# Kernel optimization log

Hardware: AMD Instinct MI355X
Metric: run time of the kernel (lower is better)

Reference implementation:

```python
import jax, jax.numpy as jnp
import numpy as np

N = 2048
VOTE_THRESH = 0.65
SOFT_TH = 0.05      # INFERENCE_TH in the original
MAX_DET = 100       # cfg.TEST.DETECTIONS_PER_IMAGE
NUM_CLASSES = 80


def setup_inputs() -> dict:
    key = jax.random.key(0)
    k1, k2, k3, k4 = jax.random.split(key, 4)
    xy = jax.random.uniform(k1, (N, 2), dtype=jnp.float32) * 800.0
    wh = jax.random.uniform(k2, (N, 2), dtype=jnp.float32) * 196.0 + 4.0
    boxes = jnp.concatenate([xy, xy + wh], axis=1)          # valid x1y1x2y2 boxes
    scores = jax.random.uniform(k3, (N,), dtype=jnp.float32) * 0.95 + 0.05
    labels = jax.random.randint(k4, (N,), 0, NUM_CLASSES, dtype=jnp.int32)
    return {"boxes": boxes, "scores": scores, "labels": labels}


def _bbox_vote_soft(det):
    """Faithful fixed-shape version of bbox_vote(..., vote_type='soft_vote').
    det: (n, 6) = [x1, y1, x2, y2, score, label]. Returns (MAX_DET, 6) rows + valid mask."""
    n = det.shape[0]
    BUF = 2 * n + 1                      # each det yields <=1 soft row + <=1 merged row; last slot = trash
    order = jnp.argsort(-det[:, 4])
    det = det[order]
    area = (det[:, 2] - det[:, 0]) * (det[:, 3] - det[:, 1])

    def step(state, _):
        alive, buf, cnt = state
        any_alive = jnp.any(alive)
        pos = jnp.argmax(alive)          # first alive in score-sorted order == current top det
        cur = det[pos]
        xx1 = jnp.maximum(cur[0], det[:, 0])
        yy1 = jnp.maximum(cur[1], det[:, 1])
        xx2 = jnp.minimum(cur[2], det[:, 2])
        yy2 = jnp.minimum(cur[3], det[:, 3])
        inter = jnp.clip(xx2 - xx1, 0.0) * jnp.clip(yy2 - yy1, 0.0)
        iou = inter / (area[pos] + area - inter)
        merge = alive & (iou >= VOTE_THRESH)
        n_merge = merge.sum()
        s = det[:, 4]
        ms = jnp.where(merge, s, 0.0)
        wsum = ms.sum()
        wsafe = jnp.where(wsum > 0, wsum, 1.0)          # guard masked no-op iterations
        wbox = (det[:, :4] * ms[:, None]).sum(0) / wsafe  # score-weighted box merge
        maxs = jnp.max(ms)                               # max score among merged (scores > 0)
        row0 = jnp.concatenate([wbox, maxs[None], cur[5][None]])  # == single det when n_merge==1
        soft_s = s * (1.0 - iou)                         # soft-NMS decayed scores
        soft_valid = merge & (soft_s >= SOFT_TH) & (n_merge > 1)
        soft_rows = jnp.concatenate([det[:, :4], soft_s[:, None], det[:, 5:6]], axis=1)
        valid = jnp.concatenate([any_alive[None], soft_valid])
        rows = jnp.concatenate([row0[None], soft_rows], axis=0)   # (n+1, 6)
        idxs = jnp.where(valid, cnt + jnp.cumsum(valid) - 1, BUF - 1)
        buf = buf.at[idxs].set(rows)
        cnt = cnt + valid.sum()
        alive = alive & (iou < VOTE_THRESH)              # drop all merged dets
        return (alive, buf, cnt), None

    init = (jnp.ones((n,), bool), jnp.zeros((BUF, 6), det.dtype), jnp.int32(0))
    (alive, buf, cnt), _ = jax.lax.scan(step, init, None, length=n)
    res = buf[: BUF - 1]
    valid = jnp.arange(BUF - 1) < cnt
    sc = jnp.where(valid, res[:, 4], -jnp.inf)
    keep = jnp.argsort(-sc)[:MAX_DET]                    # final sort by score desc + truncate
    return res[keep], valid[keep]


def reference(boxes, scores, labels):
    labf = labels.astype(boxes.dtype)
    maxc = boxes.max() + 1.0                             # batched-NMS class-offset trick
    det = jnp.concatenate([boxes + labf[:, None] * maxc, scores[:, None], labf[:, None]], axis=1)
    out, valid = _bbox_vote_soft(det)
    ob = jnp.where(valid[:, None], out[:, :4] - out[:, 5:6] * maxc, 0.0)
    os_ = jnp.where(valid, out[:, 4], 0.0)
    ol = jnp.where(valid, out[:, 5], 0.0)
    return ob, os_, ol
```

## Files before the change

kernel.cpp:

```cpp
#include <hip/hip_runtime.h>

#define NCLS 80
#define VOTE_TH 0.65f
#define SOFT_THR 0.05f
#define MAXDET 100
#define NB 1281
#define BINBASE 31232
#define CANDCAP 512
#define SEG 21
#define LAST_Z  19
#define LAST_P  ((int)0xAAAAAABDu)

#define ST(p, v) __hip_atomic_store((p), (v), __ATOMIC_RELAXED, __HIP_MEMORY_SCOPE_AGENT)
#define LD(p)    __hip_atomic_load((p), __ATOMIC_RELAXED, __HIP_MEMORY_SCOPE_AGENT)

__device__ __forceinline__ int bin_of(unsigned int b) {
    int bin = (int)(b >> 15) - BINBASE;
    return bin < 0 ? 0 : (bin > NB - 1 ? NB - 1 : bin);
}

__global__ __launch_bounds__(256, 1) void nms_fused(
    const float* __restrict__ boxes,
    const float* __restrict__ scores,
    const int* __restrict__ labels,
    int* __restrict__ kCnt,
    float* __restrict__ sArrG,
    float* __restrict__ rows,
    float* __restrict__ out,
    int n)
{
#pragma clang fp contract(off)
    const int tid = threadIdx.x;
    const int lane = tid & 63;
    const int wave = tid >> 6;
    const int cls = blockIdx.x * 4 + wave;
    const unsigned long long lmask = (1ull << lane) - 1ull;

    __shared__ int   labLds[2048];
    __shared__ int   uidx[4][64];
    __shared__ float redmax[4];
    __shared__ int   oldSh;
    __shared__ int   cnts[NCLS];
    __shared__ int   hist[NB];
    __shared__ unsigned long long cand[CANDCAP];
    __shared__ int   ncand_sh, T_sh, K_sh, tot_sh;

    const float4* b4 = (const float4*)boxes;
    float4 v[8];
#pragma unroll
    for (int i = 0; i < 8; ++i) {
        int idx = tid + i * 256;
        v[i] = (idx < n) ? b4[idx]
                         : make_float4(-3.0e38f, -3.0e38f, -3.0e38f, -3.0e38f);
    }
    int lab[8];
#pragma unroll
    for (int i = 0; i < 8; ++i) {
        int idx = tid + i * 256;
        lab[i] = (idx < n) ? labels[idx] : -1;
    }
    float m = -3.0e38f;
#pragma unroll
    for (int i = 0; i < 8; ++i)
        m = fmaxf(m, fmaxf(fmaxf(v[i].x, v[i].y), fmaxf(v[i].z, v[i].w)));
#pragma unroll
    for (int d = 32; d; d >>= 1) m = fmaxf(m, __shfl_xor(m, d));
    if (lane == 0) redmax[wave] = m;
#pragma unroll
    for (int i = 0; i < 8; ++i) labLds[tid + i * 256] = lab[i];
    __syncthreads();

    const float maxc = fmaxf(fmaxf(redmax[0], redmax[1]),
                             fmaxf(redmax[2], redmax[3])) + 1.0f;
    const float off = (float)cls * maxc;
    const float cls_f = (float)cls;

    int myLab[32];
#pragma unroll
    for (int c = 0; c < 32; ++c) myLab[c] = labLds[c * 64 + lane];
    int k = 0;
#pragma unroll 4
    for (int c = 0; c < 32; ++c) {
        bool p = (myLab[c] == cls);
        unsigned long long b = __ballot(p);
        if (p) {
            int w = k + __popcll(b & lmask);
            if (w < 64) uidx[wave][w] = c * 64 + lane;
        }
        k += __popcll(b);
    }
    if (k > 64) k = 64;
    __syncthreads();

    float s = 0.0f;
    float4 bb = make_float4(0.f, 0.f, 0.f, 0.f);
    if (lane < k) {
        int gi = uidx[wave][lane];
        s = scores[gi];
        bb = b4[gi];
    }

    int r = 0;
#pragma unroll
    for (int j = 0; j < 64; ++j) {
        float sj = __shfl(s, j);
        r += ((sj > s) || (sj == s && j < lane)) ? 1 : 0;
    }
    float x1 = 0.f, y1 = 0.f, x2 = 0.f, y2 = 0.f;
    if (lane < k) {
        x1 = bb.x + off; y1 = bb.y + off;
        x2 = bb.z + off; y2 = bb.w + off;
    }
    int addr = r * 4;
    x1 = __int_as_float(__builtin_amdgcn_ds_permute(addr, __float_as_int(x1)));
    y1 = __int_as_float(__builtin_amdgcn_ds_permute(addr, __float_as_int(y1)));
    x2 = __int_as_float(__builtin_amdgcn_ds_permute(addr, __float_as_int(x2)));
    y2 = __int_as_float(__builtin_amdgcn_ds_permute(addr, __float_as_int(y2)));
    s  = __int_as_float(__builtin_amdgcn_ds_permute(addr, __float_as_int(s)));

    float area = (x2 - x1) * (y2 - y1);
    bool alive = lane < k;

    float* rbase = rows + cls * 64 * 6;
    float* sbase = sArrG + cls * 64;
    int lcnt = 0;
    while (true) {
        unsigned long long avm = __ballot(alive);
        if (avm == 0ull) break;
        int pos = (int)__builtin_ctzll(avm);

        float cx1 = __shfl(x1, pos), cy1 = __shfl(y1, pos);
        float cx2 = __shfl(x2, pos), cy2 = __shfl(y2, pos);
        float carea = __shfl(area, pos), cs = __shfl(s, pos);

        float xx1 = fmaxf(cx1, x1), yy1 = fmaxf(cy1, y1);
        float xx2 = fminf(cx2, x2), yy2 = fminf(cy2, y2);
        float inter = fmaxf(xx2 - xx1, 0.0f) * fmaxf(yy2 - yy1, 0.0f);
        float iou = inter / ((carea + area) - inter);

        bool merge = alive && (iou >= VOTE_TH);
        unsigned long long mb = __ballot(merge);
        int nm = __popcll(mb);

        if (nm == 1) {
            if (lane == 0) {
                float* rp = rbase + lcnt * 6;
                ST(&rp[0], (cx1 * cs) / cs);
                ST(&rp[1], (cy1 * cs) / cs);
                ST(&rp[2], (cx2 * cs) / cs);
                ST(&rp[3], (cy2 * cs) / cs);
                ST(&rp[4], cs);
                ST(&rp[5], cls_f);
                ST(&sbase[lcnt], cs);
            }
            lcnt += 1;
        } else {
            float msv = merge ? s : 0.0f;
            float w0 = msv, w1 = x1 * msv, w2 = y1 * msv, w3 = x2 * msv, w4 = y2 * msv;
#pragma unroll
            for (int d = 32; d; d >>= 1) {
                w0 += __shfl_xor(w0, d);
                w1 += __shfl_xor(w1, d);
                w2 += __shfl_xor(w2, d);
                w3 += __shfl_xor(w3, d);
                w4 += __shfl_xor(w4, d);
            }
            float soft = s * (1.0f - iou);
            bool sv = merge && (soft >= SOFT_THR);
            unsigned long long sb = __ballot(sv);
            int nsoft = __popcll(sb);
            if (lane == 0) {
                float* rp = rbase + lcnt * 6;
                ST(&rp[0], w1 / w0);
                ST(&rp[1], w2 / w0);
                ST(&rp[2], w3 / w0);
                ST(&rp[3], w4 / w0);
                ST(&rp[4], cs);
                ST(&rp[5], cls_f);
                ST(&sbase[lcnt], cs);
            }
            if (sv) {
                int wp = lcnt + 1 + __popcll(sb & lmask);
                float* rp = rbase + wp * 6;
                ST(&rp[0], x1);
                ST(&rp[1], y1);
                ST(&rp[2], x2);
                ST(&rp[3], y2);
                ST(&rp[4], soft);
                ST(&rp[5], cls_f);
                ST(&sbase[wp], soft);
            }
            lcnt += 1 + nsoft;
        }
        alive = alive && (iou < VOTE_TH);
    }

    if (lane == 0) ST(&kCnt[cls], lcnt);

    __threadfence();
    __syncthreads();
    if (tid == 0)
        oldSh = __hip_atomic_fetch_add((int*)out, 1, __ATOMIC_ACQ_REL,
                                       __HIP_MEMORY_SCOPE_AGENT);
    __syncthreads();
    const int old = oldSh;
    if (old != LAST_Z && old != LAST_P) return;

    for (int i = tid; i < 6 * MAXDET; i += 256) out[i] = 0.0f;
    if (tid < NCLS) cnts[tid] = LD(&kCnt[tid]);
    for (int i = tid; i < NB; i += 256) hist[i] = 0;
    if (tid == 0) { ncand_sh = 0; tot_sh = 0; }
    __syncthreads();

    if (tid < NCLS) atomicAdd(&tot_sh, cnts[tid]);
    float svals[20];
    {
        int ci = 0;
        for (int c = wave; c < NCLS; c += 4, ++ci) {
            float sv = 0.0f;
            if (lane < cnts[c]) {
                sv = LD(&sArrG[c * 64 + lane]);
                atomicAdd(&hist[bin_of(__float_as_uint(sv))], 1);
            }
            svals[ci] = sv;
        }
    }
    __syncthreads();

    if (tid < 64) {
        int cnt_total = tot_sh;
        int K = (cnt_total < MAXDET) ? cnt_total : MAXDET;
        if (lane == 0) K_sh = K;
        int part = 0;
        if (lane < 61) {
            int b0 = lane * SEG;
            for (int b = b0; b < b0 + SEG; ++b) part += hist[b];
        }
        int suf = part;
#pragma unroll
        for (int d = 1; d < 64; d <<= 1) {
            int vsh = __shfl_down(suf, d);
            if (lane + d < 64) suf += vsh;
        }
        unsigned long long bm = __ballot(suf >= K);
        int L = (bm != 0ull) ? (63 - __builtin_clzll(bm)) : 0;
        if (lane == L) {
            int acc = suf - part;
            int T = 0;
            for (int b = L * SEG + SEG - 1; b >= L * SEG; --b) {
                acc += hist[b];
                if (acc >= K) { T = b; break; }
            }
            T_sh = T;
        }
    }
    __syncthreads();
    const int K = K_sh;
    if (K <= 0) return;
    const int T = T_sh;

    {
        int ci = 0;
        for (int c = wave; c < NCLS; c += 4, ++ci) {
            if (lane < cnts[c]) {
                unsigned int sb = __float_as_uint(svals[ci]);
                if (bin_of(sb) >= T) {
                    int idx = c * 64 + lane;
                    int p = atomicAdd(&ncand_sh, 1);
                    if (p < CANDCAP)
                        cand[p] = ((unsigned long long)sb << 32) |
                                  (unsigned long long)(0xFFFFFFFFu - (unsigned int)idx);
                }
            }
        }
    }
    __syncthreads();

    int nc = ncand_sh; if (nc > CANDCAP) nc = CANDCAP;
    for (int j = tid; j < nc; j += 256) {
        unsigned long long my = cand[j];
        int rank = 0;
        for (int l = 0; l < nc; ++l) rank += (cand[l] > my) ? 1 : 0;
        if (rank < K) {
            int idx = (int)(0xFFFFFFFFu - (unsigned int)(my & 0xFFFFFFFFull));
            float* rp = rows + idx * 6;
            float r0 = LD(&rp[0]);
            float r1 = LD(&rp[1]);
            float r2 = LD(&rp[2]);
            float r3 = LD(&rp[3]);
            float r4 = LD(&rp[4]);
            float lb = LD(&rp[5]);
            float o = lb * maxc;
            out[rank * 4 + 0] = r0 - o;
            out[rank * 4 + 1] = r1 - o;
            out[rank * 4 + 2] = r2 - o;
            out[rank * 4 + 3] = r3 - o;
            out[4 * MAXDET + rank] = r4;
            out[5 * MAXDET + rank] = lb;
        }
    }
}

extern "C" void kernel_launch(void* const* d_in, const int* in_sizes, int n_in,
                              void* d_out, int out_size, void* d_ws, size_t ws_size,
                              hipStream_t stream) {
    const float* boxes  = (const float*)d_in[0];
    const float* scores = (const float*)d_in[1];
    const int*   labels = (const int*)d_in[2];
    float* out = (float*)d_out;
    const int n = in_sizes[1];

    char* ws = (char*)d_ws;
    int*   kCnt  = (int*)(ws + 0);
    float* sArrG = (float*)(ws + 512);
    float* rows  = (float*)(ws + 512 + 20480);

    hipLaunchKernelGGL(nms_fused, dim3(NCLS / 4), dim3(256), 0, stream,
                       boxes, scores, labels, kCnt, sArrG, rows, out, n);
}
```

Measured before the change: 92.47 us.

## Stage per-class rows in LDS and pre-select per-block top-100 before global merge

Vote output rows and scores are now written to shared memory instead of global workspace with per-element atomic stores. Each block then ranks its own 256 candidates locally and publishes only its top 100 keys plus packed 64-bit row data to global memory. The last block reads these compact keys directly, avoiding per-class count loads and scattered row fetches. This adds a local 256-way rank pass per block and changes the workspace layout.

```diff
diff --git a/kernel.cpp b/kernel.cpp
--- a/kernel.cpp
+++ b/kernel.cpp
@@ -8,24 +8,30 @@
 #define BINBASE 31232
 #define CANDCAP 512
 #define SEG 21
+#define NBLK 20
 #define LAST_Z  19
 #define LAST_P  ((int)0xAAAAAABDu)
 
-#define ST(p, v) __hip_atomic_store((p), (v), __ATOMIC_RELAXED, __HIP_MEMORY_SCOPE_AGENT)
-#define LD(p)    __hip_atomic_load((p), __ATOMIC_RELAXED, __HIP_MEMORY_SCOPE_AGENT)
+#define STU(p, v) __hip_atomic_store((p), (v), __ATOMIC_RELAXED, __HIP_MEMORY_SCOPE_AGENT)
+#define LDU(p)    __hip_atomic_load((p), __ATOMIC_RELAXED, __HIP_MEMORY_SCOPE_AGENT)
+
+typedef unsigned long long u64;
 
 __device__ __forceinline__ int bin_of(unsigned int b) {
     int bin = (int)(b >> 15) - BINBASE;
     return bin < 0 ? 0 : (bin > NB - 1 ? NB - 1 : bin);
 }
+__device__ __forceinline__ u64 packf(float a, float b) {
+    return (u64)__float_as_uint(a) | ((u64)__float_as_uint(b) << 32);
+}
 
 __global__ __launch_bounds__(256, 1) void nms_fused(
     const float* __restrict__ boxes,
     const float* __restrict__ scores,
     const int* __restrict__ labels,
-    int* __restrict__ kCnt,
-    float* __restrict__ sArrG,
-    float* __restrict__ rows,
+    u64* __restrict__ keyG,
+    u64* __restrict__ candG,
+    int* __restrict__ rowTot,
     float* __restrict__ out,
     int n)
 {
@@ -39,10 +45,14 @@
     __shared__ int   labLds[2048];
     __shared__ int   uidx[4][64];
     __shared__ float redmax[4];
+    __shared__ float rowsL[4 * 64 * 6];
+    __shared__ float sL[4 * 64];
+    __shared__ int   lcntL[4];
+    __shared__ u64   keysL[256];
     __shared__ int   oldSh;
-    __shared__ int   cnts[NCLS];
     __shared__ int   hist[NB];
-    __shared__ unsigned long long cand[CANDCAP];
+    __shared__ u64   cand[CANDCAP];
+    __shared__ short candPos[CANDCAP];
     __shared__ int   ncand_sh, T_sh, K_sh, tot_sh;
 
     const float4* b4 = (const float4*)boxes;
@@ -121,8 +131,8 @@
     float area = (x2 - x1) * (y2 - y1);
     bool alive = lane < k;
 
-    float* rbase = rows + cls * 64 * 6;
-    float* sbase = sArrG + cls * 64;
+    float* rbase = rowsL + wave * 64 * 6;
+    float* sbase = sL + wave * 64;
     int lcnt = 0;
     while (true) {
         unsigned long long avm = __ballot(alive);
@@ -145,13 +155,10 @@
         if (nm == 1) {
             if (lane == 0) {
                 float* rp = rbase + lcnt * 6;
-                ST(&rp[0], (cx1 * cs) / cs);
-                ST(&rp[1], (cy1 * cs) / cs);
-                ST(&rp[2], (cx2 * cs) / cs);
-                ST(&rp[3], (cy2 * cs) / cs);
-                ST(&rp[4], cs);
-                ST(&rp[5], cls_f);
-                ST(&sbase[lcnt], cs);
+                rp[0] = (cx1 * cs) / cs; rp[1] = (cy1 * cs) / cs;
+                rp[2] = (cx2 * cs) / cs; rp[3] = (cy2 * cs) / cs;
+                rp[4] = cs; rp[5] = cls_f;
+                sbase[lcnt] = cs;
             }
             lcnt += 1;
         } else {
@@ -171,31 +178,49 @@
             int nsoft = __popcll(sb);
             if (lane == 0) {
                 float* rp = rbase + lcnt * 6;
-                ST(&rp[0], w1 / w0);
-                ST(&rp[1], w2 / w0);
-                ST(&rp[2], w3 / w0);
-                ST(&rp[3], w4 / w0);
-                ST(&rp[4], cs);
-                ST(&rp[5], cls_f);
-                ST(&sbase[lcnt], cs);
+                rp[0] = w1 / w0; rp[1] = w2 / w0;
+                rp[2] = w3 / w0; rp[3] = w4 / w0;
+                rp[4] = cs; rp[5] = cls_f;
+                sbase[lcnt] = cs;
             }
             if (sv) {
                 int wp = lcnt + 1 + __popcll(sb & lmask);
                 float* rp = rbase + wp * 6;
-                ST(&rp[0], x1);
-                ST(&rp[1], y1);
-                ST(&rp[2], x2);
-                ST(&rp[3], y2);
-                ST(&rp[4], soft);
-                ST(&rp[5], cls_f);
-                ST(&sbase[wp], soft);
+                rp[0] = x1; rp[1] = y1; rp[2] = x2; rp[3] = y2;
+                rp[4] = soft; rp[5] = cls_f;
+                sbase[wp] = soft;
             }
             lcnt += 1 + nsoft;
         }
         alive = alive && (iou < VOTE_TH);
     }
-
-    if (lane == 0) ST(&kCnt[cls], lcnt);
+    if (lane == 0) lcntL[wave] = lcnt;
+    __syncthreads();
+
+    const int nvalid = lcntL[0] + lcntL[1] + lcntL[2] + lcntL[3];
+    const bool valid = lane < lcntL[wave];
+    u64 mykey = 0ull;
+    if (valid) {
+        unsigned int sb = __float_as_uint(sL[wave * 64 + lane]);
+        int gidx = cls * 64 + lane;
+        mykey = ((u64)sb << 32) | (u64)(0xFFFFFFFFu - (unsigned int)gidx);
+    }
+    keysL[tid] = mykey;
+    __syncthreads();
+    int lrank = 0;
+    for (int j = 0; j < 256; ++j)
+        lrank += (keysL[j] > mykey) ? 1 : 0;
+    if (valid && lrank < 100) {
+        int base = blockIdx.x * 100 + lrank;
+        const float* rp = rowsL + (wave * 64 + lane) * 6;
+        STU(&keyG[base], mykey);
+        STU(&candG[base * 3 + 0], packf(rp[0], rp[1]));
+        STU(&candG[base * 3 + 1], packf(rp[2], rp[3]));
+        STU(&candG[base * 3 + 2], packf(rp[4], rp[5]));
+    }
+    if (tid >= nvalid && tid < 100)
+        STU(&keyG[blockIdx.x * 100 + tid], 0ull);
+    if (tid == 0) STU(&rowTot[blockIdx.x], nvalid);
 
     __threadfence();
     __syncthreads();
@@ -207,24 +232,21 @@
     if (old != LAST_Z && old != LAST_P) return;
 
     for (int i = tid; i < 6 * MAXDET; i += 256) out[i] = 0.0f;
-    if (tid < NCLS) cnts[tid] = LD(&kCnt[tid]);
     for (int i = tid; i < NB; i += 256) hist[i] = 0;
     if (tid == 0) { ncand_sh = 0; tot_sh = 0; }
-    __syncthreads();
-
-    if (tid < NCLS) atomicAdd(&tot_sh, cnts[tid]);
-    float svals[20];
-    {
-        int ci = 0;
-        for (int c = wave; c < NCLS; c += 4, ++ci) {
-            float sv = 0.0f;
-            if (lane < cnts[c]) {
-                sv = LD(&sArrG[c * 64 + lane]);
-                atomicAdd(&hist[bin_of(__float_as_uint(sv))], 1);
-            }
-            svals[ci] = sv;
-        }
-    }
+    u64 kv[8];
+#pragma unroll
+    for (int ii = 0; ii < 8; ++ii) {
+        int j = tid + ii * 256;
+        kv[ii] = (j < NBLK * 100) ? LDU(&keyG[j]) : 0ull;
+    }
+    int bt = (tid < NBLK) ? LDU(&rowTot[tid]) : 0;
+    __syncthreads();
+    if (tid < NBLK) atomicAdd(&tot_sh, bt);
+#pragma unroll
+    for (int ii = 0; ii < 8; ++ii)
+        if (kv[ii] != 0ull)
+            atomicAdd(&hist[bin_of((unsigned int)(kv[ii] >> 32))], 1);
     __syncthreads();
 
     if (tid < 64) {
@@ -259,18 +281,14 @@
     if (K <= 0) return;
     const int T = T_sh;
 
-    {
-        int ci = 0;
-        for (int c = wave; c < NCLS; c += 4, ++ci) {
-            if (lane < cnts[c]) {
-                unsigned int sb = __float_as_uint(svals[ci]);
-                if (bin_of(sb) >= T) {
-                    int idx = c * 64 + lane;
-                    int p = atomicAdd(&ncand_sh, 1);
-                    if (p < CANDCAP)
-                        cand[p] = ((unsigned long long)sb << 32) |
-                                  (unsigned long long)(0xFFFFFFFFu - (unsigned int)idx);
-                }
+#pragma unroll
+    for (int ii = 0; ii < 8; ++ii) {
+        if (kv[ii] != 0ull &&
+            bin_of((unsigned int)(kv[ii] >> 32)) >= T) {
+            int p = atomicAdd(&ncand_sh, 1);
+            if (p < CANDCAP) {
+                cand[p] = kv[ii];
+                candPos[p] = (short)(tid + ii * 256);
             }
         }
     }
@@ -278,18 +296,20 @@
 
     int nc = ncand_sh; if (nc > CANDCAP) nc = CANDCAP;
     for (int j = tid; j < nc; j += 256) {
-        unsigned long long my = cand[j];
+        u64 my = cand[j];
         int rank = 0;
         for (int l = 0; l < nc; ++l) rank += (cand[l] > my) ? 1 : 0;
         if (rank < K) {
-            int idx = (int)(0xFFFFFFFFu - (unsigned int)(my & 0xFFFFFFFFull));
-            float* rp = rows + idx * 6;
-            float r0 = LD(&rp[0]);
-            float r1 = LD(&rp[1]);
-            float r2 = LD(&rp[2]);
-            float r3 = LD(&rp[3]);
-            float r4 = LD(&rp[4]);
-            float lb = LD(&rp[5]);
+            int pos = (int)candPos[j];
+            u64 u0 = LDU(&candG[pos * 3 + 0]);
+            u64 u1 = LDU(&candG[pos * 3 + 1]);
+            u64 u2 = LDU(&candG[pos * 3 + 2]);
+            float r0 = __uint_as_float((unsigned int)(u0 & 0xFFFFFFFFull));
+            float r1 = __uint_as_float((unsigned int)(u0 >> 32));
+            float r2 = __uint_as_float((unsigned int)(u1 & 0xFFFFFFFFull));
+            float r3 = __uint_as_float((unsigned int)(u1 >> 32));
+            float r4 = __uint_as_float((unsigned int)(u2 & 0xFFFFFFFFull));
+            float lb = __uint_as_float((unsigned int)(u2 >> 32));
             float o = lb * maxc;
             out[rank * 4 + 0] = r0 - o;
             out[rank * 4 + 1] = r1 - o;
@@ -311,10 +331,10 @@
     const int n = in_sizes[1];
 
     char* ws = (char*)d_ws;
-    int*   kCnt  = (int*)(ws + 0);
-    float* sArrG = (float*)(ws + 512);
-    float* rows  = (float*)(ws + 512 + 20480);
-
-    hipLaunchKernelGGL(nms_fused, dim3(NCLS / 4), dim3(256), 0, stream,
-                       boxes, scores, labels, kCnt, sArrG, rows, out, n);
+    u64* keyG   = (u64*)(ws + 0);
+    u64* candG  = (u64*)(ws + 16384);
+    int* rowTot = (int*)(ws + 16384 + 49152);
+
+    hipLaunchKernelGGL(nms_fused, dim3(NBLK), dim3(256), 0, stream,
+                       boxes, scores, labels, keyG, candG, rowTot, out, n);
 }
```

After: 85.68 us. 1.08x faster.
